# Kernel optimization log

Measured on AMD Instinct MI355X. Metric: run time of the kernel, lower is better.

The kernel has to match this reference:

```python
import jax, jax.numpy as jnp
import numpy as np

DIMS = [1024, 2048, 2048, 51]
B, P = 16, 1024


def setup_inputs() -> dict:
    key = jax.random.key(0)
    ks = jax.random.split(key, 1 + 2 * (len(DIMS) - 1))
    inp = {
        "num_pairs": P,
        "classifier_input": jax.random.normal(ks[0], (B, P, DIMS[0]), dtype=jnp.float32),
        "num_batches": B,
    }
    # Linear params, PyTorch-style: W[out, in], b[out]
    for li in range(len(DIMS) - 1):
        fan_in = DIMS[li]
        bound = 1.0 / np.sqrt(fan_in)
        inp[f"W{li}"] = jax.random.uniform(ks[1 + 2 * li], (DIMS[li + 1], fan_in), minval=-bound, maxval=bound, dtype=jnp.float32)
        inp[f"b{li}"] = jax.random.uniform(ks[2 + 2 * li], (DIMS[li + 1],), minval=-bound, maxval=bound, dtype=jnp.float32)
    return inp


def reference(num_pairs, classifier_input, num_batches, W0, b0, W1, b1, W2, b2):
    # Batched MLP over all (num_batches * num_pairs) vectors at once.
    # Original loops per (b, i); math is identical. dropout p=0.0 -> identity.
    x = classifier_input  # [B, P, d_in]
    x = jax.nn.relu(jnp.einsum("bpd,hd->bph", x, W0) + b0)
    x = jax.nn.relu(jnp.einsum("bpd,hd->bph", x, W1) + b1)
    out = jnp.einsum("bpd,od->bpo", x, W2) + b2  # [B, P, n_classes]
    return out
```

## Files before the change

kernel.cpp:

```cpp
#include <hip/hip_runtime.h>
#include <hip/hip_bf16.h>
#include <stdint.h>

typedef __attribute__((ext_vector_type(8))) short short8;
typedef __attribute__((ext_vector_type(8))) uint16_t ushort8;
typedef __attribute__((ext_vector_type(4))) float floatx4;

#define TK 32


__device__ __forceinline__ uint16_t f2bf_bits(float f) {
    uint32_t u = __builtin_bit_cast(uint32_t, f);
    u += 0x7FFFu + ((u >> 16) & 1u);
    return (uint16_t)(u >> 16);
}

__device__ __forceinline__ void async_copy16(const void* g, void* l) {
    auto gp = (const __attribute__((address_space(1))) uint32_t*)(uintptr_t)g;
    auto lp = (__attribute__((address_space(3))) uint32_t*)(uint32_t)(uintptr_t)l;
    __builtin_amdgcn_global_load_lds(gp, lp, 16, 0, 0);
}


__global__ void cvt8(const float* __restrict__ src, uint16_t* __restrict__ dst, int n) {
    int i = (blockIdx.x * 256 + threadIdx.x) * 8;
    if (i >= n) return;
    floatx4 a = *(const floatx4*)(src + i);
    floatx4 b = *(const floatx4*)(src + i + 4);
    ushort8 o;
#pragma unroll
    for (int k = 0; k < 4; k++) {
        o[k]     = f2bf_bits(a[k]);
        o[k + 4] = f2bf_bits(b[k]);
    }
    *(ushort8*)(dst + i) = o;
}

__global__ void cvt_pad_w2(const float* __restrict__ src, uint16_t* __restrict__ dst) {
    int i = (blockIdx.x * 256 + threadIdx.x) * 8;
    int row = i >> 11;
    ushort8 o;
    if (row < 51) {
        floatx4 a = *(const floatx4*)(src + i);
        floatx4 b = *(const floatx4*)(src + i + 4);
#pragma unroll
        for (int k = 0; k < 4; k++) {
            o[k]     = f2bf_bits(a[k]);
            o[k + 4] = f2bf_bits(b[k]);
        }
    } else {
#pragma unroll
        for (int k = 0; k < 8; k++) o[k] = 0;
    }
    *(ushort8*)(dst + i) = o;
}


template <int MI, int NJ, bool RELU, bool OUTF32>
__global__ __launch_bounds__(256, 2)
void gemm_bt(const uint16_t* __restrict__ A,
             const uint16_t* __restrict__ W,
             const float* __restrict__ bias,
             void* __restrict__ out,
             int M, int N, int K, int ldc, int nstore)
{
    constexpr int TMv = MI * 32;
    constexpr int TNv = NJ * 32;
    constexpr int ACH = MI / 2;
    constexpr int NCH = NJ / 2;

    __shared__ alignas(16) uint16_t sA[TMv * TK];
    __shared__ alignas(16) uint16_t sB[TNv * TK];

    const int tid  = threadIdx.x;
    const int wave = tid >> 6;
    const int lane = tid & 63;
    const int n0 = blockIdx.x * TNv;
    const int m0 = blockIdx.y * TMv;

    floatx4 acc[MI][NJ];
    const floatx4 zero = {0.f, 0.f, 0.f, 0.f};
#pragma unroll
    for (int i = 0; i < MI; i++)
#pragma unroll
        for (int j = 0; j < NJ; j++) acc[i][j] = zero;

    const int wr = (wave >> 1) * MI * 16;
    const int wc = (wave & 1) * NJ * 16;

    const int lr = lane >> 2;
    const int lc = (lane & 3) * 8;

    const uint16_t* ap[ACH];
    const uint16_t* bp[NCH];
#pragma unroll
    for (int t = 0; t < ACH; t++)
        ap[t] = A + (size_t)(m0 + (wave + 4 * t) * 16 + lr) * K + lc;
#pragma unroll
    for (int t = 0; t < NCH; t++)
        bp[t] = W + (size_t)(n0 + (wave + 4 * t) * 16 + lr) * K + lc;

    const int fm = lane & 15;
    const int fk = (lane >> 4) * 8;

    const int niter = K / TK;
    for (int it = 0; it < niter; it++) {
#pragma unroll
        for (int t = 0; t < ACH; t++) {
            async_copy16(ap[t], sA + (wave + 4 * t) * 512);
            ap[t] += TK;
        }
#pragma unroll
        for (int t = 0; t < NCH; t++) {
            async_copy16(bp[t], sB + (wave + 4 * t) * 512);
            bp[t] += TK;
        }
        __syncthreads();

        short8 af[MI], bfr[NJ];
#pragma unroll
        for (int i = 0; i < MI; i++)
            af[i] = *(const short8*)(sA + (wr + i * 16 + fm) * TK + fk);
#pragma unroll
        for (int j = 0; j < NJ; j++)
            bfr[j] = *(const short8*)(sB + (wc + j * 16 + fm) * TK + fk);
#pragma unroll
        for (int i = 0; i < MI; i++)
#pragma unroll
            for (int j = 0; j < NJ; j++)
                acc[i][j] = __builtin_amdgcn_mfma_f32_16x16x32_bf16(af[i], bfr[j], acc[i][j], 0, 0, 0);
        __syncthreads();
    }

    const int cr = (lane >> 4) * 4;
    const int cc = lane & 15;
#pragma unroll
    for (int i = 0; i < MI; i++) {
        const int gmb = m0 + wr + i * 16 + cr;
#pragma unroll
        for (int j = 0; j < NJ; j++) {
            const int gn = n0 + wc + j * 16 + cc;
            if (gn < nstore) {
                const float bv = bias[gn];
#pragma unroll
                for (int r = 0; r < 4; r++) {
                    float v = acc[i][j][r] + bv;
                    if (RELU) v = fmaxf(v, 0.f);
                    const size_t idx = (size_t)(gmb + r) * ldc + gn;
                    if (OUTF32) ((float*)out)[idx] = v;
                    else        ((uint16_t*)out)[idx] = f2bf_bits(v);
                }
            }
        }
    }
}


extern "C" void kernel_launch(void* const* d_in, const int* in_sizes, int n_in,
                              void* d_out, int out_size, void* d_ws, size_t ws_size,
                              hipStream_t stream) {
    (void)in_sizes; (void)n_in; (void)out_size; (void)ws_size;
    const float* X  = (const float*)d_in[1];
    const float* W0 = (const float*)d_in[3];
    const float* b0 = (const float*)d_in[4];
    const float* W1 = (const float*)d_in[5];
    const float* b1 = (const float*)d_in[6];
    const float* W2 = (const float*)d_in[7];
    const float* b2 = (const float*)d_in[8];

    const int M = 16384;

    char* w = (char*)d_ws;
    uint16_t* X0  = (uint16_t*)w; w += (size_t)M * 1024 * 2;
    uint16_t* X1  = (uint16_t*)w; w += (size_t)M * 2048 * 2;
    uint16_t* X2  = (uint16_t*)w; w += (size_t)M * 2048 * 2;
    uint16_t* W0b = (uint16_t*)w; w += (size_t)2048 * 1024 * 2;
    uint16_t* W1b = (uint16_t*)w; w += (size_t)2048 * 2048 * 2;
    uint16_t* W2b = (uint16_t*)w; w += (size_t)128 * 2048 * 2;

    cvt8<<<M * 1024 / 8 / 256, 256, 0, stream>>>(X, X0, M * 1024);
    cvt8<<<2048 * 1024 / 8 / 256, 256, 0, stream>>>(W0, W0b, 2048 * 1024);
    cvt8<<<2048 * 2048 / 8 / 256, 256, 0, stream>>>(W1, W1b, 2048 * 2048);
    cvt_pad_w2<<<128 * 2048 / 8 / 256, 256, 0, stream>>>(W2, W2b);

    gemm_bt<4, 8, true, false><<<dim3(2048 / 256, M / 128), 256, 0, stream>>>(
        X0, W0b, b0, X1, M, 2048, 1024, 2048, 2048);
    gemm_bt<4, 8, true, false><<<dim3(2048 / 256, M / 128), 256, 0, stream>>>(
        X1, W1b, b1, X2, M, 2048, 2048, 2048, 2048);
    gemm_bt<2, 4, false, true><<<dim3(1, M / 64), 256, 0, stream>>>(
        X2, W2b, b2, d_out, M, 128, 2048, 51, 51);
}
```

Before: 419.7 us.

## Double K-tile, add XOR-swizzled LDS layout, XCD-aware block mapping, shrink final layer padding

Raises the K step per iteration from 32 to 64, halving barrier count per K, and stores A/B tiles in LDS with an XOR swizzle so fragment reads avoid bank conflicts. Switches to a 1-D grid remapped so each XCD works on a contiguous band of M rows, which should improve L2 reuse of activation rows. The last layer pads W2 to 64 rows instead of 128 and uses smaller 32x64 tiles to cut wasted MMA work. LDS per block doubles, which may reduce occupancy.

```diff
diff --git a/kernel.cpp b/kernel.cpp
--- a/kernel.cpp
+++ b/kernel.cpp
@@ -6,7 +6,7 @@
 typedef __attribute__((ext_vector_type(8))) uint16_t ushort8;
 typedef __attribute__((ext_vector_type(4))) float floatx4;
 
-#define TK 32
+#define TK 64
 
 
 __device__ __forceinline__ uint16_t f2bf_bits(float f) {
@@ -66,8 +66,8 @@
 {
     constexpr int TMv = MI * 32;
     constexpr int TNv = NJ * 32;
-    constexpr int ACH = MI / 2;
-    constexpr int NCH = NJ / 2;
+    constexpr int ACH = TMv / 32;
+    constexpr int BCH = TNv / 32;
 
     __shared__ alignas(16) uint16_t sA[TMv * TK];
     __shared__ alignas(16) uint16_t sB[TNv * TK];
@@ -75,8 +75,16 @@
     const int tid  = threadIdx.x;
     const int wave = tid >> 6;
     const int lane = tid & 63;
-    const int n0 = blockIdx.x * TNv;
-    const int m0 = blockIdx.y * TMv;
+
+    const int f   = blockIdx.x;
+    const int xcd = f & 7;
+    const int loc = f >> 3;
+    const int per = (int)gridDim.x >> 3;
+    const int nt  = N / TNv;
+    const int n_t = loc % nt;
+    const int m_t = xcd * (per / nt) + loc / nt;
+    const int n0 = n_t * TNv;
+    const int m0 = m_t * TMv;
 
     floatx4 acc[MI][NJ];
     const floatx4 zero = {0.f, 0.f, 0.f, 0.f};
@@ -88,20 +96,21 @@
     const int wr = (wave >> 1) * MI * 16;
     const int wc = (wave & 1) * NJ * 16;
 
-    const int lr = lane >> 2;
-    const int lc = (lane & 3) * 8;
+    const int sr   = lane >> 3;
+    const int scol = ((lane & 7) ^ sr) * 8;
 
     const uint16_t* ap[ACH];
-    const uint16_t* bp[NCH];
+    const uint16_t* bp[BCH];
 #pragma unroll
     for (int t = 0; t < ACH; t++)
-        ap[t] = A + (size_t)(m0 + (wave + 4 * t) * 16 + lr) * K + lc;
-#pragma unroll
-    for (int t = 0; t < NCH; t++)
-        bp[t] = W + (size_t)(n0 + (wave + 4 * t) * 16 + lr) * K + lc;
+        ap[t] = A + (size_t)(m0 + (wave + 4 * t) * 8 + sr) * K + scol;
+#pragma unroll
+    for (int t = 0; t < BCH; t++)
+        bp[t] = W + (size_t)(n0 + (wave + 4 * t) * 8 + sr) * K + scol;
 
     const int fm = lane & 15;
-    const int fk = (lane >> 4) * 8;
+    const int fr = fm & 7;
+    const int kgb = lane >> 4;
 
     const int niter = K / TK;
     for (int it = 0; it < niter; it++) {
@@ -111,24 +120,28 @@
             ap[t] += TK;
         }
 #pragma unroll
-        for (int t = 0; t < NCH; t++) {
+        for (int t = 0; t < BCH; t++) {
             async_copy16(bp[t], sB + (wave + 4 * t) * 512);
             bp[t] += TK;
         }
         __syncthreads();
 
-        short8 af[MI], bfr[NJ];
-#pragma unroll
-        for (int i = 0; i < MI; i++)
-            af[i] = *(const short8*)(sA + (wr + i * 16 + fm) * TK + fk);
-#pragma unroll
-        for (int j = 0; j < NJ; j++)
-            bfr[j] = *(const short8*)(sB + (wc + j * 16 + fm) * TK + fk);
-#pragma unroll
-        for (int i = 0; i < MI; i++)
+#pragma unroll
+        for (int kk = 0; kk < 2; kk++) {
+            const int slot = ((kgb + 4 * kk) ^ fr) * 8;
+            short8 af[MI], bfr[NJ];
+#pragma unroll
+            for (int i = 0; i < MI; i++)
+                af[i] = *(const short8*)(sA + (wr + i * 16 + fm) * TK + slot);
 #pragma unroll
             for (int j = 0; j < NJ; j++)
-                acc[i][j] = __builtin_amdgcn_mfma_f32_16x16x32_bf16(af[i], bfr[j], acc[i][j], 0, 0, 0);
+                bfr[j] = *(const short8*)(sB + (wc + j * 16 + fm) * TK + slot);
+#pragma unroll
+            for (int i = 0; i < MI; i++)
+#pragma unroll
+                for (int j = 0; j < NJ; j++)
+                    acc[i][j] = __builtin_amdgcn_mfma_f32_16x16x32_bf16(af[i], bfr[j], acc[i][j], 0, 0, 0);
+        }
         __syncthreads();
     }
 
@@ -176,17 +189,17 @@
     uint16_t* X2  = (uint16_t*)w; w += (size_t)M * 2048 * 2;
     uint16_t* W0b = (uint16_t*)w; w += (size_t)2048 * 1024 * 2;
     uint16_t* W1b = (uint16_t*)w; w += (size_t)2048 * 2048 * 2;
-    uint16_t* W2b = (uint16_t*)w; w += (size_t)128 * 2048 * 2;
+    uint16_t* W2b = (uint16_t*)w; w += (size_t)64 * 2048 * 2;
 
     cvt8<<<M * 1024 / 8 / 256, 256, 0, stream>>>(X, X0, M * 1024);
     cvt8<<<2048 * 1024 / 8 / 256, 256, 0, stream>>>(W0, W0b, 2048 * 1024);
     cvt8<<<2048 * 2048 / 8 / 256, 256, 0, stream>>>(W1, W1b, 2048 * 2048);
-    cvt_pad_w2<<<128 * 2048 / 8 / 256, 256, 0, stream>>>(W2, W2b);
-
-    gemm_bt<4, 8, true, false><<<dim3(2048 / 256, M / 128), 256, 0, stream>>>(
+    cvt_pad_w2<<<64 * 2048 / 8 / 256, 256, 0, stream>>>(W2, W2b);
+
+    gemm_bt<4, 8, true, false><<<dim3((M / 128) * (2048 / 256)), 256, 0, stream>>>(
         X0, W0b, b0, X1, M, 2048, 1024, 2048, 2048);
-    gemm_bt<4, 8, true, false><<<dim3(2048 / 256, M / 128), 256, 0, stream>>>(
+    gemm_bt<4, 8, true, false><<<dim3((M / 128) * (2048 / 256)), 256, 0, stream>>>(
         X1, W1b, b1, X2, M, 2048, 2048, 2048, 2048);
-    gemm_bt<2, 4, false, true><<<dim3(1, M / 64), 256, 0, stream>>>(
-        X2, W2b, b2, d_out, M, 128, 2048, 51, 51);
-}
+    gemm_bt<1, 2, false, true><<<dim3(M / 32), 256, 0, stream>>>(
+        X2, W2b, b2, d_out, M, 64, 2048, 51, 51);
+}
```

New measurement: 347.6 us. -17.2%, faster.
